# Kernel optimization log

Measured on AMD Instinct MI355X. Metric: run time of the kernel, lower is better.

The kernel has to match this reference:

```python
import jax, jax.numpy as jnp
import numpy as np

COST_CLASS = 1.0
COST_BBOX = 1.0
COST_GIOU = 1.0
COST_MASK_CE = 1.0
COST_MASK_DICE = 1.0
ALPHA = 0.25   # hardcoded in forward (focal alpha)
GAMMA = 2.0


def box_cxcywh_to_xyxy(b):
    cx, cy, w, h = jnp.split(b, 4, axis=-1)
    return jnp.concatenate([cx - 0.5 * w, cy - 0.5 * h, cx + 0.5 * w, cy + 0.5 * h], axis=-1)


def generalized_box_iou(b1, b2):
    # b1 [N,4], b2 [M,4] in xyxy -> [N,M]
    a1 = (b1[:, 2] - b1[:, 0]) * (b1[:, 3] - b1[:, 1])
    a2 = (b2[:, 2] - b2[:, 0]) * (b2[:, 3] - b2[:, 1])
    lt = jnp.maximum(b1[:, None, :2], b2[None, :, :2])
    rb = jnp.minimum(b1[:, None, 2:], b2[None, :, 2:])
    wh = jnp.clip(rb - lt, 0.0)
    inter = wh[..., 0] * wh[..., 1]
    union = a1[:, None] + a2[None, :] - inter
    iou = inter / union
    ltc = jnp.minimum(b1[:, None, :2], b2[None, :, :2])
    rbc = jnp.maximum(b1[:, None, 2:], b2[None, :, 2:])
    whc = jnp.clip(rbc - ltc, 0.0)
    area = whc[..., 0] * whc[..., 1]
    return iou - (area - union) / area


def point_sample_bilinear(masks, coords):
    # masks [N,H,W], coords [P,2] in [0,1] (x,y); grid_sample align_corners=False,
    # zero padding: pixel = coord*size - 0.5. Fully batched over N and P.
    H, W = masks.shape[-2:]
    x = coords[:, 0] * W - 0.5
    y = coords[:, 1] * H - 0.5
    x0 = jnp.floor(x); y0 = jnp.floor(y)
    wx = x - x0; wy = y - y0
    x0i = x0.astype(jnp.int32); y0i = y0.astype(jnp.int32)
    def g(yi, xi):
        valid = ((xi >= 0) & (xi < W) & (yi >= 0) & (yi < H)).astype(masks.dtype)
        v = masks[:, jnp.clip(yi, 0, H - 1), jnp.clip(xi, 0, W - 1)]  # [N,P]
        return v * valid
    return (g(y0i, x0i) * (1 - wy) * (1 - wx) + g(y0i, x0i + 1) * (1 - wy) * wx
            + g(y0i + 1, x0i) * wy * (1 - wx) + g(y0i + 1, x0i + 1) * wy * wx)


def point_sample_nearest(masks, coords):
    H, W = masks.shape[-2:]
    xi = jnp.round(coords[:, 0] * W - 0.5).astype(jnp.int32)
    yi = jnp.round(coords[:, 1] * H - 0.5).astype(jnp.int32)
    valid = ((xi >= 0) & (xi < W) & (yi >= 0) & (yi < H)).astype(masks.dtype)
    return masks[:, jnp.clip(yi, 0, H - 1), jnp.clip(xi, 0, W - 1)] * valid


def _cost_single(logits, boxes, labels, tboxes, pmasks, tmasks, pts):
    # logits [Q,C], boxes [Q,4], labels [T], tboxes [T,4],
    # pmasks [Q,H,W], tmasks [T,H,W] (0/1 int), pts [P,2]
    prob = jax.nn.sigmoid(logits)
    neg_cost = (1 - ALPHA) * prob ** GAMMA * (-jax.nn.log_sigmoid(-logits))
    pos_cost = ALPHA * (1 - prob) ** GAMMA * (-jax.nn.log_sigmoid(logits))
    cost_class = jnp.take(pos_cost, labels, axis=1) - jnp.take(neg_cost, labels, axis=1)  # [Q,T]
    giou = generalized_box_iou(box_cxcywh_to_xyxy(boxes), box_cxcywh_to_xyxy(tboxes))
    cost_bbox = jnp.abs(boxes[:, None, :] - tboxes[None, :, :]).sum(-1)  # L1 cdist
    C = COST_BBOX * cost_bbox + COST_CLASS * cost_class - COST_GIOU * giou
    # batched point sampling (replaces per-query / per-target python loops)
    pm = point_sample_bilinear(pmasks, pts)                    # [Q,P]
    tm = point_sample_nearest(tmasks.astype(pmasks.dtype), pts)  # [T,P]
    P = pm.shape[-1]
    # batch_sigmoid_ce_loss: pairwise BCE-with-logits, mean over points
    pos_ce = jax.nn.softplus(-pm)  # loss if target==1
    neg_ce = jax.nn.softplus(pm)   # loss if target==0
    ce = (pos_ce @ tm.T + neg_ce @ (1.0 - tm).T) / P
    # batch_dice_loss
    sm = jax.nn.sigmoid(pm)
    num = 2.0 * (sm @ tm.T)
    den = sm.sum(-1)[:, None] + tm.sum(-1)[None, :]
    dice = 1.0 - (num + 1.0) / (den + 1.0)
    C = C + COST_MASK_CE * ce + COST_MASK_DICE * dice
    # replicate C[C.isinf()|C.isnan()] = 2*max
    finite = jnp.isfinite(C)
    mx = jnp.max(jnp.where(finite, C, -jnp.inf))
    return jnp.where(finite, C, 2.0 * mx)


def setup_inputs() -> dict:
    key = jax.random.key(0)
    ks = jax.random.split(key, 7)
    bs, Q, C, T, H, W = 2, 900, 91, 100, 128, 128
    P = H * W // 16  # mask_point_sample_ratio = 16
    return {
        "pred_logits": jax.random.normal(ks[0], (bs, Q, C), jnp.float32),
        "pred_boxes": jax.random.uniform(ks[1], (bs, Q, 4), jnp.float32),
        "tgt_labels": jax.random.randint(ks[2], (bs, T), 0, C, jnp.int32),
        "tgt_boxes": jax.random.uniform(ks[3], (bs, T, 4), jnp.float32),
        "pred_masks": jax.random.normal(ks[4], (bs, Q, H, W), jnp.float32),
        "tgt_masks": jax.random.randint(ks[5], (bs, T, H, W), 0, 2, jnp.int32),
        "point_coords": jax.random.uniform(ks[6], (bs, P, 2), jnp.float32),
    }


def reference(pred_logits, pred_boxes, tgt_labels, tgt_boxes, pred_masks, tgt_masks, point_coords):
    # Returns the per-image matching cost matrices [bs, Q, T]; the CPU-side
    # Hungarian solve (scipy linear_sum_assignment) consumes these.
    return jax.vmap(_cost_single)(pred_logits, pred_boxes, tgt_labels, tgt_boxes,
                                  pred_masks, tgt_masks, point_coords)
```

## Files before the change

kernel.cpp:

```cpp
#include <hip/hip_runtime.h>
#include <math.h>

#define QN 900
#define TN 100
#define CN 91
#define PN 1024
#define HWD 128
#define BS 2

typedef float f32x2 __attribute__((ext_vector_type(2)));

__device__ __forceinline__ float sigmoidf_(float x) {
    return 1.0f / (1.0f + __expf(-x));
}
__device__ __forceinline__ float softplusf_(float x) {
    return fmaxf(x, 0.0f) + __logf(1.0f + __expf(-fabsf(x)));
}
__device__ __forceinline__ unsigned bfhi(float f) {
    unsigned u = __float_as_uint(f);
    return (u + 0x7FFFu + ((u >> 16) & 1u)) & 0xFFFF0000u;
}

__global__ __launch_bounds__(1024) void sort_kernel(
    const float2* __restrict__ coords, uint4* __restrict__ table)
{
    __shared__ int whist[16][HWD];
    __shared__ int woff[16][HWD];
    __shared__ int rowtot[HWD];
    __shared__ int rowbase[HWD];
    __shared__ unsigned short perm[PN];

    const int b = blockIdx.x;
    const int tid = threadIdx.x;
    const int wv = tid >> 6, lane = tid & 63;

    ((int*)whist)[tid] = 0;
    ((int*)whist)[tid + 1024] = 0;
    __syncthreads();

    float2 cd = coords[b * PN + tid];
    float yf = cd.y * (float)HWD - 0.5f;
    int y0 = (int)floorf(yf);
    const int r = min(max(y0, 0), HWD - 1);

    int rank = 0;
    for (int j = 0; j < 64; ++j) {
        int rj = __shfl(r, j);
        rank += (j < lane) & (rj == r);
    }
    atomicAdd(&whist[wv][r], 1);
    __syncthreads();

    if (tid < HWD) {
        int acc = 0;
#pragma unroll
        for (int w = 0; w < 16; ++w) { woff[w][tid] = acc; acc += whist[w][tid]; }
        rowtot[tid] = acc;
    }
    __syncthreads();
    if (tid == 0) {
        int acc = 0;
        for (int rr = 0; rr < HWD; ++rr) { rowbase[rr] = acc; acc += rowtot[rr]; }
    }
    __syncthreads();

    const int slot = rowbase[r] + woff[wv][r] + rank;
    perm[slot] = (unsigned short)tid;
    __syncthreads();

    const int idx = (int)perm[tid];
    cd = coords[b * PN + idx];
    float x = cd.x * (float)HWD - 0.5f;
    float y = cd.y * (float)HWD - 0.5f;
    float fx = floorf(x), fy = floorf(y);
    int x0 = (int)fx;
    int py0 = (int)fy;
    int py1 = py0 + 1;
    float wx = x - fx, wy = y - fy;
    bool bx0, bx1;
    int xl;
    if (x0 < 0)             { xl = 0;       bx0 = true;  bx1 = false; wx = 1.f - wx; }
    else if (x0 >= HWD - 1) { xl = HWD - 2; bx0 = false; bx1 = true;  wx = 1.f - wx; }
    else                    { xl = x0;      bx0 = true;  bx1 = true; }
    bool by0 = (py0 >= 0) & (py0 < HWD);
    bool by1 = (py1 >= 0) & (py1 < HWD);
    int yc0 = min(max(py0, 0), HWD - 1), yc1 = min(max(py1, 0), HWD - 1);
    unsigned ar0 = (unsigned)(yc0 * HWD + xl);
    unsigned ar1 = (unsigned)(yc1 * HWD + xl);
    unsigned fl = (unsigned)bx0 | ((unsigned)bx1 << 1) |
                  ((unsigned)by0 << 2) | ((unsigned)by1 << 3);
    int xi = (int)rintf(cd.x * (float)HWD - 0.5f);
    int yi = (int)rintf(cd.y * (float)HWD - 0.5f);
    unsigned nvalid = (xi >= 0) & (xi < HWD) & (yi >= 0) & (yi < HWD);
    unsigned naddr = (unsigned)(min(max(yi, 0), HWD - 1) * HWD + min(max(xi, 0), HWD - 1));

    uint4 te;
    te.x = ar0 | (ar1 << 14) | (fl << 28);
    te.y = __float_as_uint(wx);
    te.z = __float_as_uint(wy);
    te.w = naddr | (nvalid << 14);
    table[b * PN + tid] = te;
}

__global__ __launch_bounds__(256) void prep_kernel(
    const uint4* __restrict__ table, const int* __restrict__ tmasks,
    unsigned* __restrict__ tmw, float* __restrict__ tmsum)
{
    __shared__ int cnt[4];
    const int bx = blockIdx.x;
    const int tid = threadIdx.x;
    const int wv = tid >> 6, lane = tid & 63;
    const int b = bx / TN, t = bx % TN;
    const int* m = tmasks + (size_t)(b * TN + t) * (HWD * HWD);
    int addr[4]; unsigned vld[4];
#pragma unroll
    for (int c = 0; c < 4; ++c) {
        unsigned w = table[b * PN + c * 256 + tid].w;
        addr[c] = (int)(w & 16383u);
        vld[c] = w >> 14;
    }
    int rv[4];
#pragma unroll
    for (int c = 0; c < 4; ++c) rv[c] = m[addr[c]];
    int mycnt = 0;
#pragma unroll
    for (int c = 0; c < 4; ++c) {
        unsigned long long bal = __ballot(vld[c] && (rv[c] != 0));
        if (lane == 0) {
            tmw[(size_t)(b * TN + t) * 32 + c * 8 + wv * 2 + 0] = (unsigned)(bal & 0xFFFFFFFFull);
            tmw[(size_t)(b * TN + t) * 32 + c * 8 + wv * 2 + 1] = (unsigned)(bal >> 32);
            mycnt += __popcll(bal);
        }
    }
    if (lane == 0) cnt[wv] = mycnt;
    __syncthreads();
    if (tid == 0)
        tmsum[b * TN + t] = (float)((cnt[0] + cnt[1]) + (cnt[2] + cnt[3]));
}

__global__ __launch_bounds__(256, 4) void main_kernel(
    const float* __restrict__ logits, const float4* __restrict__ pboxes,
    const int* __restrict__ labels, const float4* __restrict__ tboxes,
    const float* __restrict__ pmasks, const uint4* __restrict__ table,
    const unsigned* __restrict__ tmw, const float* __restrict__ tmsum_,
    float* __restrict__ out, float* __restrict__ blockmax,
    int* __restrict__ badflag)
{
    __shared__ unsigned pl[PN];
    __shared__ float part[8][32][9];
    __shared__ float sred[8];
    __shared__ float mred[256];
    __shared__ int sbad;

    const int bq = blockIdx.x;
    const int b = bq / QN, q = bq - b * QN;
    const int tid = threadIdx.x;
    const int wv = tid >> 6, lane = tid & 63;
    const int pc = tid >> 5, ts = tid & 31;
    const float* mask = pmasks + (size_t)bq * (HWD * HWD);

    if (tid == 0) sbad = 0;

    unsigned fl[4];
    float wxa[4], wya[4];
    int ar0[4], ar1[4];
#pragma unroll
    for (int c = 0; c < 4; ++c) {
        uint4 te = table[b * PN + c * 256 + tid];
        ar0[c] = (int)(te.x & 16383u);
        ar1[c] = (int)((te.x >> 14) & 16383u);
        fl[c] = te.x >> 28;
        wxa[c] = __uint_as_float(te.y);
        wya[c] = __uint_as_float(te.z);
    }

    f32x2 p0[4], p1[4];
#pragma unroll
    for (int c = 0; c < 4; ++c) {
        p0[c] = *(const f32x2*)(mask + ar0[c]);
        p1[c] = *(const f32x2*)(mask + ar1[c]);
    }

    const unsigned* rowb = tmw + (size_t)b * TN * 32;
    unsigned w0[4], w1[4], w2[4], w3[4];
#pragma unroll
    for (int g = 0; g < 4; ++g) {
        w0[g] = rowb[(ts +  0) * 32 + pc * 4 + g];
        w1[g] = rowb[(ts + 32) * 32 + pc * 4 + g];
        w2[g] = rowb[(ts + 64) * 32 + pc * 4 + g];
        w3[g] = (ts + 96 < TN) ? rowb[(ts + 96) * 32 + pc * 4 + g] : 0u;
    }
    float lg = 0.f, tsum = 0.f;
    float4 tb = make_float4(0, 0, 0, 0), pb = make_float4(0, 0, 0, 0);
    if (tid < TN) {
        int lab = labels[b * TN + tid];
        lg = logits[(size_t)(b * QN + q) * CN + lab];
        tsum = tmsum_[b * TN + tid];
        tb = tboxes[b * TN + tid];
        pb = pboxes[b * QN + q];
    }

    float lsp = 0.f, lsm = 0.f;
#pragma unroll
    for (int c = 0; c < 4; ++c) {
        const bool bx0 = fl[c] & 1u, bx1 = fl[c] & 2u, by0 = fl[c] & 4u, by1 = fl[c] & 8u;
        float v00 = (by0 && bx0) ? p0[c].x : 0.f;
        float v01 = (by0 && bx1) ? p0[c].y : 0.f;
        float v10 = (by1 && bx0) ? p1[c].x : 0.f;
        float v11 = (by1 && bx1) ? p1[c].y : 0.f;
        float wx = wxa[c], wy = wya[c];
        float pm = (v00 * (1.f - wx) + v01 * wx) * (1.f - wy) +
                   (v10 * (1.f - wx) + v11 * wx) * wy;
        float sg = sigmoidf_(pm);
        lsp += softplusf_(pm);
        lsm += sg;
        pl[c * 256 + tid] = bfhi(pm) | (bfhi(sg) >> 16);
    }
    for (int off = 32; off > 0; off >>= 1) {
        lsp += __shfl_down(lsp, off);
        lsm += __shfl_down(lsm, off);
    }
    if (lane == 0) { sred[wv * 2 + 0] = lsp; sred[wv * 2 + 1] = lsm; }
    __syncthreads();
    float s_sp = (sred[0] + sred[2]) + (sred[4] + sred[6]);
    float s_sm = (sred[1] + sred[3]) + (sred[5] + sred[7]);

    float a0 = 0, a1 = 0, a2 = 0, a3 = 0, a4 = 0, a5 = 0, a6 = 0, a7 = 0;
#pragma unroll
    for (int g = 0; g < 4; ++g) {
        unsigned u0 = w0[g], u1 = w1[g], u2 = w2[g], u3 = w3[g];
        int p0i = pc * 128 + g * 32;
#pragma unroll
        for (int jj = 0; jj < 8; ++jj) {
            uint4 u = *(const uint4*)&pl[p0i + jj * 4];
#pragma unroll
            for (int k = 0; k < 4; ++k) {
                unsigned uv = (k == 0) ? u.x : (k == 1) ? u.y : (k == 2) ? u.z : u.w;
                float pmv = __uint_as_float(uv & 0xFFFF0000u);
                float sgv = __uint_as_float(uv << 16);
                float f0 = (float)((u0 >> k) & 1u);
                float f1 = (float)((u1 >> k) & 1u);
                float f2 = (float)((u2 >> k) & 1u);
                float f3 = (float)((u3 >> k) & 1u);
                a0 = fmaf(pmv, f0, a0); a1 = fmaf(sgv, f0, a1);
                a2 = fmaf(pmv, f1, a2); a3 = fmaf(sgv, f1, a3);
                a4 = fmaf(pmv, f2, a4); a5 = fmaf(sgv, f2, a5);
                a6 = fmaf(pmv, f3, a6); a7 = fmaf(sgv, f3, a7);
            }
            u0 >>= 4; u1 >>= 4; u2 >>= 4; u3 >>= 4;
        }
    }
    part[pc][ts][0] = a0; part[pc][ts][1] = a1;
    part[pc][ts][2] = a2; part[pc][ts][3] = a3;
    part[pc][ts][4] = a4; part[pc][ts][5] = a5;
    part[pc][ts][6] = a6; part[pc][ts][7] = a7;
    __syncthreads();

    float val = -INFINITY;
    if (tid < TN) {
        int t = tid, tss = t & 31, kk = t >> 5;
        float apm = 0.f, asg = 0.f;
#pragma unroll
        for (int pp = 0; pp < 8; ++pp) {
            apm += part[pp][tss][kk * 2 + 0];
            asg += part[pp][tss][kk * 2 + 1];
        }
        float ce = (s_sp - apm) * (1.0f / (float)PN);
        float dice = 1.0f - (2.0f * asg + 1.0f) / (s_sm + tsum + 1.0f);

        float pr = sigmoidf_(lg);
        float cls = 0.25f * (1.f - pr) * (1.f - pr) * softplusf_(-lg)
                  - 0.75f * pr * pr * softplusf_(lg);

        float l1 = fabsf(pb.x - tb.x) + fabsf(pb.y - tb.y) +
                   fabsf(pb.z - tb.z) + fabsf(pb.w - tb.w);

        float px1 = pb.x - 0.5f * pb.z, py1 = pb.y - 0.5f * pb.w;
        float px2 = pb.x + 0.5f * pb.z, py2 = pb.y + 0.5f * pb.w;
        float tx1 = tb.x - 0.5f * tb.z, ty1 = tb.y - 0.5f * tb.w;
        float tx2 = tb.x + 0.5f * tb.z, ty2 = tb.y + 0.5f * tb.w;
        float A1 = (px2 - px1) * (py2 - py1);
        float A2 = (tx2 - tx1) * (ty2 - ty1);
        float iw = fmaxf(fminf(px2, tx2) - fmaxf(px1, tx1), 0.f);
        float ih = fmaxf(fminf(py2, ty2) - fmaxf(py1, ty1), 0.f);
        float inter = iw * ih;
        float uni = A1 + A2 - inter;
        float iou = inter / uni;
        float cw = fmaxf(fmaxf(px2, tx2) - fminf(px1, tx1), 0.f);
        float chh = fmaxf(fmaxf(py2, ty2) - fminf(py1, ty1), 0.f);
        float area = cw * chh;
        float giou = iou - (area - uni) / area;

        float Cv = l1 + cls - giou + ce + dice;
        out[(size_t)(b * QN + q) * TN + t] = Cv;
        if (isfinite(Cv)) val = Cv;
        else sbad = 1;
    }
    mred[tid] = val;
    __syncthreads();
    if (tid < 64) {
        float m = fmaxf(fmaxf(mred[tid], mred[tid + 64]),
                        fmaxf(mred[tid + 128], mred[tid + 192]));
        for (int off = 32; off > 0; off >>= 1)
            m = fmaxf(m, __shfl_down(m, off));
        if (tid == 0) { blockmax[bq] = m; badflag[bq] = sbad; }
    }
}

__global__ __launch_bounds__(128) void fix_kernel(float* __restrict__ out,
                                                  const float* __restrict__ blockmax,
                                                  const int* __restrict__ badflag)
{
    const int bq = blockIdx.x;
    if (badflag[bq] == 0) return;
    const int tid = threadIdx.x;
    if (tid >= TN) return;
    const int b = bq / QN;
    float v = out[(size_t)bq * TN + tid];
    if (!isfinite(v)) {
        float m = -INFINITY;
        for (int k = 0; k < QN; ++k) m = fmaxf(m, blockmax[b * QN + k]);
        out[(size_t)bq * TN + tid] = 2.0f * m;
    }
}

extern "C" void kernel_launch(void* const* d_in, const int* in_sizes, int n_in,
                              void* d_out, int out_size, void* d_ws, size_t ws_size,
                              hipStream_t stream) {
    const float* logits  = (const float*)d_in[0];
    const float4* pboxes = (const float4*)d_in[1];
    const int* labels    = (const int*)d_in[2];
    const float4* tboxes = (const float4*)d_in[3];
    const float* pmasks  = (const float*)d_in[4];
    const int* tmasks    = (const int*)d_in[5];
    const float* coords  = (const float*)d_in[6];
    float* out = (float*)d_out;

    char* ws = (char*)d_ws;
    unsigned* tmw   = (unsigned*)(ws);
    float* tmsum    = (float*)(ws + 25600);
    float* blockmax = (float*)(ws + 26400);
    int* badflag    = (int*)(ws + 33600);
    uint4* table    = (uint4*)(ws + 40960);

    hipLaunchKernelGGL(sort_kernel, dim3(BS), dim3(1024), 0, stream,
                       (const float2*)coords, table);
    hipLaunchKernelGGL(prep_kernel, dim3(BS * TN), dim3(256), 0, stream,
                       table, tmasks, tmw, tmsum);
    hipLaunchKernelGGL(main_kernel, dim3(BS * QN), dim3(256), 0, stream,
                       logits, pboxes, labels, tboxes, pmasks, table,
                       tmw, tmsum, out, blockmax, badflag);
    hipLaunchKernelGGL(fix_kernel, dim3(BS * QN), dim3(128), 0, stream,
                       out, blockmax, badflag);
}
```

Measured before the change: 53.40 us.

## Merge coordinate sort and target-mask prep into one launch

Combines the sort kernel and the target-mask prep kernel into a single launch. The first blocks build the row-sorted sample table, and the remaining blocks sample the target masks in original point order, so prep no longer depends on the sorted table. The main kernel now writes each point's packed prediction value to its original index, which keeps it aligned with the unsorted target bitmasks. The aim is to remove one kernel launch and the serial dependency between sort and prep. In exchange, the main kernel's shared-memory writes become scattered.

```diff
diff --git a/kernel.cpp b/kernel.cpp
--- a/kernel.cpp
+++ b/kernel.cpp
@@ -21,8 +21,10 @@
     return (u + 0x7FFFu + ((u >> 16) & 1u)) & 0xFFFF0000u;
 }
 
-__global__ __launch_bounds__(1024) void sort_kernel(
-    const float2* __restrict__ coords, uint4* __restrict__ table)
+__global__ __launch_bounds__(1024) void combo_kernel(
+    const float2* __restrict__ coords, const int* __restrict__ tmasks,
+    uint4* __restrict__ table, unsigned* __restrict__ tmw,
+    float* __restrict__ tmsum)
 {
     __shared__ int whist[16][HWD];
     __shared__ int woff[16][HWD];
@@ -30,112 +32,99 @@
     __shared__ int rowbase[HWD];
     __shared__ unsigned short perm[PN];
 
-    const int b = blockIdx.x;
-    const int tid = threadIdx.x;
-    const int wv = tid >> 6, lane = tid & 63;
-
-    ((int*)whist)[tid] = 0;
-    ((int*)whist)[tid + 1024] = 0;
-    __syncthreads();
-
-    float2 cd = coords[b * PN + tid];
-    float yf = cd.y * (float)HWD - 0.5f;
-    int y0 = (int)floorf(yf);
-    const int r = min(max(y0, 0), HWD - 1);
-
-    int rank = 0;
-    for (int j = 0; j < 64; ++j) {
-        int rj = __shfl(r, j);
-        rank += (j < lane) & (rj == r);
-    }
-    atomicAdd(&whist[wv][r], 1);
-    __syncthreads();
-
-    if (tid < HWD) {
-        int acc = 0;
-#pragma unroll
-        for (int w = 0; w < 16; ++w) { woff[w][tid] = acc; acc += whist[w][tid]; }
-        rowtot[tid] = acc;
-    }
-    __syncthreads();
-    if (tid == 0) {
-        int acc = 0;
-        for (int rr = 0; rr < HWD; ++rr) { rowbase[rr] = acc; acc += rowtot[rr]; }
-    }
-    __syncthreads();
-
-    const int slot = rowbase[r] + woff[wv][r] + rank;
-    perm[slot] = (unsigned short)tid;
-    __syncthreads();
-
-    const int idx = (int)perm[tid];
-    cd = coords[b * PN + idx];
-    float x = cd.x * (float)HWD - 0.5f;
-    float y = cd.y * (float)HWD - 0.5f;
-    float fx = floorf(x), fy = floorf(y);
-    int x0 = (int)fx;
-    int py0 = (int)fy;
-    int py1 = py0 + 1;
-    float wx = x - fx, wy = y - fy;
-    bool bx0, bx1;
-    int xl;
-    if (x0 < 0)             { xl = 0;       bx0 = true;  bx1 = false; wx = 1.f - wx; }
-    else if (x0 >= HWD - 1) { xl = HWD - 2; bx0 = false; bx1 = true;  wx = 1.f - wx; }
-    else                    { xl = x0;      bx0 = true;  bx1 = true; }
-    bool by0 = (py0 >= 0) & (py0 < HWD);
-    bool by1 = (py1 >= 0) & (py1 < HWD);
-    int yc0 = min(max(py0, 0), HWD - 1), yc1 = min(max(py1, 0), HWD - 1);
-    unsigned ar0 = (unsigned)(yc0 * HWD + xl);
-    unsigned ar1 = (unsigned)(yc1 * HWD + xl);
-    unsigned fl = (unsigned)bx0 | ((unsigned)bx1 << 1) |
-                  ((unsigned)by0 << 2) | ((unsigned)by1 << 3);
-    int xi = (int)rintf(cd.x * (float)HWD - 0.5f);
-    int yi = (int)rintf(cd.y * (float)HWD - 0.5f);
-    unsigned nvalid = (xi >= 0) & (xi < HWD) & (yi >= 0) & (yi < HWD);
-    unsigned naddr = (unsigned)(min(max(yi, 0), HWD - 1) * HWD + min(max(xi, 0), HWD - 1));
-
-    uint4 te;
-    te.x = ar0 | (ar1 << 14) | (fl << 28);
-    te.y = __float_as_uint(wx);
-    te.z = __float_as_uint(wy);
-    te.w = naddr | (nvalid << 14);
-    table[b * PN + tid] = te;
-}
-
-__global__ __launch_bounds__(256) void prep_kernel(
-    const uint4* __restrict__ table, const int* __restrict__ tmasks,
-    unsigned* __restrict__ tmw, float* __restrict__ tmsum)
-{
-    __shared__ int cnt[4];
     const int bx = blockIdx.x;
     const int tid = threadIdx.x;
     const int wv = tid >> 6, lane = tid & 63;
-    const int b = bx / TN, t = bx % TN;
-    const int* m = tmasks + (size_t)(b * TN + t) * (HWD * HWD);
-    int addr[4]; unsigned vld[4];
-#pragma unroll
-    for (int c = 0; c < 4; ++c) {
-        unsigned w = table[b * PN + c * 256 + tid].w;
-        addr[c] = (int)(w & 16383u);
-        vld[c] = w >> 14;
-    }
-    int rv[4];
-#pragma unroll
-    for (int c = 0; c < 4; ++c) rv[c] = m[addr[c]];
-    int mycnt = 0;
-#pragma unroll
-    for (int c = 0; c < 4; ++c) {
-        unsigned long long bal = __ballot(vld[c] && (rv[c] != 0));
+
+    if (bx < BS) {
+        const int b = bx;
+        ((int*)whist)[tid] = 0;
+        ((int*)whist)[tid + 1024] = 0;
+        __syncthreads();
+
+        float2 cd = coords[b * PN + tid];
+        float yf = cd.y * (float)HWD - 0.5f;
+        int y0k = (int)floorf(yf);
+        const int r = min(max(y0k, 0), HWD - 1);
+
+        int rank = 0;
+        for (int j = 0; j < 64; ++j) {
+            int rj = __shfl(r, j);
+            rank += (j < lane) & (rj == r);
+        }
+        atomicAdd(&whist[wv][r], 1);
+        __syncthreads();
+
+        if (tid < HWD) {
+            int acc = 0;
+#pragma unroll
+            for (int w = 0; w < 16; ++w) { woff[w][tid] = acc; acc += whist[w][tid]; }
+            rowtot[tid] = acc;
+        }
+        __syncthreads();
+        if (tid == 0) {
+            int acc = 0;
+            for (int rr = 0; rr < HWD; ++rr) { rowbase[rr] = acc; acc += rowtot[rr]; }
+        }
+        __syncthreads();
+
+        const int slot = rowbase[r] + woff[wv][r] + rank;
+        perm[slot] = (unsigned short)tid;
+        __syncthreads();
+
+        const int idx = (int)perm[tid];
+        cd = coords[b * PN + idx];
+        float x = cd.x * (float)HWD - 0.5f;
+        float y = cd.y * (float)HWD - 0.5f;
+        float fx = floorf(x), fy = floorf(y);
+        int x0 = (int)fx;
+        int py0 = (int)fy;
+        int py1 = py0 + 1;
+        float wx = x - fx, wy = y - fy;
+        bool bx0, bx1;
+        int xl;
+        if (x0 < 0)             { xl = 0;       bx0 = true;  bx1 = false; wx = 1.f - wx; }
+        else if (x0 >= HWD - 1) { xl = HWD - 2; bx0 = false; bx1 = true;  wx = 1.f - wx; }
+        else                    { xl = x0;      bx0 = true;  bx1 = true; }
+        bool by0 = (py0 >= 0) & (py0 < HWD);
+        bool by1 = (py1 >= 0) & (py1 < HWD);
+        int yc0 = min(max(py0, 0), HWD - 1), yc1 = min(max(py1, 0), HWD - 1);
+        unsigned ar0 = (unsigned)(yc0 * HWD + xl);
+        unsigned ar1 = (unsigned)(yc1 * HWD + xl);
+        unsigned fl = (unsigned)bx0 | ((unsigned)bx1 << 1) |
+                      ((unsigned)by0 << 2) | ((unsigned)by1 << 3);
+        uint4 te;
+        te.x = ar0 | (ar1 << 14) | (fl << 28);
+        te.y = __float_as_uint(wx);
+        te.z = __float_as_uint(wy);
+        te.w = (unsigned)idx;
+        table[b * PN + tid] = te;
+    } else {
+        const int bt = bx - BS;
+        const int b = bt / TN, t = bt % TN;
+        const int* m = tmasks + (size_t)(b * TN + t) * (HWD * HWD);
+        int* cnt = (int*)whist;
+
+        float2 cd = coords[b * PN + tid];
+        int xi = (int)rintf(cd.x * (float)HWD - 0.5f);
+        int yi = (int)rintf(cd.y * (float)HWD - 0.5f);
+        unsigned vld = (xi >= 0) & (xi < HWD) & (yi >= 0) & (yi < HWD);
+        int addr = min(max(yi, 0), HWD - 1) * HWD + min(max(xi, 0), HWD - 1);
+        int rv = m[addr];
+        unsigned long long bal = __ballot(vld && (rv != 0));
         if (lane == 0) {
-            tmw[(size_t)(b * TN + t) * 32 + c * 8 + wv * 2 + 0] = (unsigned)(bal & 0xFFFFFFFFull);
-            tmw[(size_t)(b * TN + t) * 32 + c * 8 + wv * 2 + 1] = (unsigned)(bal >> 32);
-            mycnt += __popcll(bal);
-        }
-    }
-    if (lane == 0) cnt[wv] = mycnt;
-    __syncthreads();
-    if (tid == 0)
-        tmsum[b * TN + t] = (float)((cnt[0] + cnt[1]) + (cnt[2] + cnt[3]));
+            tmw[(size_t)(b * TN + t) * 32 + wv * 2 + 0] = (unsigned)(bal & 0xFFFFFFFFull);
+            tmw[(size_t)(b * TN + t) * 32 + wv * 2 + 1] = (unsigned)(bal >> 32);
+            cnt[wv] = __popcll(bal);
+        }
+        __syncthreads();
+        if (tid == 0) {
+            int acc = 0;
+#pragma unroll
+            for (int w = 0; w < 16; ++w) acc += cnt[w];
+            tmsum[b * TN + t] = (float)acc;
+        }
+    }
 }
 
 __global__ __launch_bounds__(256, 4) void main_kernel(
@@ -161,7 +150,7 @@
 
     if (tid == 0) sbad = 0;
 
-    unsigned fl[4];
+    unsigned fl[4], orig[4];
     float wxa[4], wya[4];
     int ar0[4], ar1[4];
 #pragma unroll
@@ -172,6 +161,7 @@
         fl[c] = te.x >> 28;
         wxa[c] = __uint_as_float(te.y);
         wya[c] = __uint_as_float(te.z);
+        orig[c] = te.w;
     }
 
     f32x2 p0[4], p1[4];
@@ -214,7 +204,7 @@
         float sg = sigmoidf_(pm);
         lsp += softplusf_(pm);
         lsm += sg;
-        pl[c * 256 + tid] = bfhi(pm) | (bfhi(sg) >> 16);
+        pl[orig[c]] = bfhi(pm) | (bfhi(sg) >> 16);
     }
     for (int off = 32; off > 0; off >>= 1) {
         lsp += __shfl_down(lsp, off);
@@ -343,10 +333,8 @@
     int* badflag    = (int*)(ws + 33600);
     uint4* table    = (uint4*)(ws + 40960);
 
-    hipLaunchKernelGGL(sort_kernel, dim3(BS), dim3(1024), 0, stream,
-                       (const float2*)coords, table);
-    hipLaunchKernelGGL(prep_kernel, dim3(BS * TN), dim3(256), 0, stream,
-                       table, tmasks, tmw, tmsum);
+    hipLaunchKernelGGL(combo_kernel, dim3(BS + BS * TN), dim3(1024), 0, stream,
+                       (const float2*)coords, tmasks, table, tmw, tmsum);
     hipLaunchKernelGGL(main_kernel, dim3(BS * QN), dim3(256), 0, stream,
                        logits, pboxes, labels, tboxes, pmasks, table,
                        tmw, tmsum, out, blockmax, badflag);
```

Result: faster. 50.02 us, median of 2 (-6.3%).
